# Optimization experiments

Hardware: AMD Instinct MI355X
Metric: run time of the kernel (lower is better)

The kernel has to match this reference:

```python
import jax, jax.numpy as jnp
import numpy as np
from jax import lax

NPOINT = 1024
NSAMPLE = 32
BN_EPS = 1e-3  # keras BatchNormalization default epsilon


def _fps(xyz, npoint):
    # Farthest point sampling. Matches the TF loop: the NEW farthest index is
    # recorded at each step (the initial index-0 seed is never recorded).
    B, N, _ = xyz.shape

    def step(carry, _):
        dist, far = carry
        centroid = jnp.take_along_axis(xyz, far[:, None, None], axis=1)  # (B,1,3)
        d2 = jnp.sum(jnp.square(xyz - centroid), axis=-1)  # (B,N)
        dist = jnp.minimum(dist, d2)
        nf = jnp.argmax(dist, axis=-1).astype(jnp.int32)
        return (dist, nf), nf

    init = (jnp.full((B, N), 1e10, dtype=xyz.dtype), jnp.zeros((B,), jnp.int32))
    _, idxs = lax.scan(step, init, None, length=npoint)
    return jnp.transpose(idxs)  # (B, npoint)


def _pairwise_d2(a, b):
    # a: (B,S,3), b: (B,N,3) -> (B,S,N) squared distances
    a2 = jnp.sum(a * a, axis=-1, keepdims=True)
    b2 = jnp.sum(b * b, axis=-1, keepdims=True)
    ab = jnp.einsum('bsc,bnc->bsn', a, b)
    return jnp.maximum(a2 - 2.0 * ab + jnp.swapaxes(b2, 1, 2), 0.0)


def _forward(xyz, features, params):
    fps_idx = _fps(xyz, NPOINT)  # (B,S)
    new_xyz = jnp.take_along_axis(xyz, fps_idx[..., None], axis=1)  # (B,S,3)
    d2 = _pairwise_d2(new_xyz, xyz)  # (B,S,N)
    _, idx = lax.top_k(-d2, NSAMPLE)  # (B,S,K) knn indices
    gather = jax.vmap(lambda p, i: p[i])  # per-batch gather
    grouped_xyz = gather(xyz, idx) - new_xyz[:, :, None, :]  # (B,S,K,3)
    grouped_feat = gather(features, idx)  # (B,S,K,C)
    x = jnp.concatenate([grouped_xyz, grouped_feat], axis=-1)
    for W, b, g, be, m, v in params:
        # Conv2D(kernel=1, activation='relu') then BatchNormalization (inference)
        x = jax.nn.relu(jnp.einsum('bskc,cd->bskd', x, W) + b)
        x = g * (x - m) * lax.rsqrt(v + BN_EPS) + be
    return new_xyz, jnp.max(x, axis=2)  # (B,S,3), (B,S,C_out)


def setup_inputs() -> dict:
    key = jax.random.key(0)
    ks = jax.random.split(key, 16)
    B, N, CF = 16, 4096, 64
    mlp = [64, 64, 128]
    inp = {
        'xyz': jax.random.normal(ks[0], (B, N, 3), jnp.float32),
        'features': jax.random.normal(ks[1], (B, N, CF), jnp.float32),
    }
    c = 3 + CF
    ki = 2
    for li, co in enumerate(mlp):
        inp[f'W{li}'] = jax.random.normal(ks[ki], (c, co), jnp.float32) * 0.05; ki += 1
        inp[f'b{li}'] = jnp.zeros((co,), jnp.float32)
        inp[f'g{li}'] = 1.0 + 0.02 * jax.random.normal(ks[ki], (co,), jnp.float32); ki += 1
        inp[f'be{li}'] = 0.02 * jax.random.normal(ks[ki], (co,), jnp.float32); ki += 1
        inp[f'm{li}'] = jnp.zeros((co,), jnp.float32)
        inp[f'v{li}'] = jnp.ones((co,), jnp.float32)
        c = co
    return inp


def reference(xyz, features, W0, b0, g0, be0, m0, v0, W1, b1, g1, be1, m1, v1, W2, b2, g2, be2, m2, v2):
    params = [(W0, b0, g0, be0, m0, v0), (W1, b1, g1, be1, m1, v1), (W2, b2, g2, be2, m2, v2)]
    return _forward(xyz, features, params)
```

## Files before the change

kernel.cpp:

```cpp
#include <hip/hip_runtime.h>

#define NB 16
#define NPTS 4096
#define NS 1024
#define NK 32
#define NCF 64


#define F_INF __int_as_float(0x7f800000)

#define DPP_SHR1   0x111
#define DPP_SHR2   0x112
#define DPP_SHR4   0x114
#define DPP_SHR8   0x118
#define DPP_BCAST15 0x142
#define DPP_BCAST31 0x143

#define DPP_MAX_STEP(cur, CTRL) do{ \
  int lo_=__builtin_amdgcn_update_dpp((int)(unsigned)(cur),(int)(unsigned)(cur),CTRL,0xF,0xF,false); \
  int hi_=__builtin_amdgcn_update_dpp((int)(unsigned)((cur)>>32),(int)(unsigned)((cur)>>32),CTRL,0xF,0xF,false); \
  unsigned long long nk_=(((unsigned long long)(unsigned)hi_)<<32)|(unsigned)lo_; \
  if (nk_>(cur)) (cur)=nk_; \
}while(0)

__global__ __launch_bounds__(256, 2) void fps_kernel(
  const float* __restrict__ xyz, float* __restrict__ out)
{
  __shared__ float sxyz[NPTS*3];
  __shared__ unsigned long long skey[2][4];
  __shared__ int sfps[NS];
  const int b = blockIdx.x, tid = threadIdx.x;
  const float* bp = xyz + (size_t)b*NPTS*3;

  {
    const float4* src=(const float4*)bp;
    float4* dst=(float4*)sxyz;
    for (int i=tid;i<NPTS*3/4;i+=256) dst[i]=src[i];
  }
  float px[16],py[16],pz[16],dist[16];
  #pragma unroll
  for (int r=0;r<16;r++){
    int p=r*256+tid;
    px[r]=bp[p*3]; py[r]=bp[p*3+1]; pz[r]=bp[p*3+2];
    dist[r]=1e10f;
  }
  __syncthreads();
  int far=0;
  for (int s=0;s<NS;++s){
    float cx=sxyz[far*3],cy=sxyz[far*3+1],cz=sxyz[far*3+2];
    float bv=-1.0f; int bslot=0;
    #pragma unroll
    for (int r=0;r<16;r++){
      float dx=__fsub_rn(px[r],cx);
      float dy=__fsub_rn(py[r],cy);
      float dz=__fsub_rn(pz[r],cz);
      float d2=__fadd_rn(__fadd_rn(__fmul_rn(dx,dx),__fmul_rn(dy,dy)),__fmul_rn(dz,dz));
      float nd=fminf(dist[r],d2);
      dist[r]=nd;
      if (nd>bv){bv=nd;bslot=r;}
    }
    int bidx=bslot*256+tid;
    unsigned long long cur=(((unsigned long long)__float_as_uint(bv))<<32)
                           |(unsigned)(4095-bidx);
    DPP_MAX_STEP(cur,DPP_SHR1);
    DPP_MAX_STEP(cur,DPP_SHR2);
    DPP_MAX_STEP(cur,DPP_SHR4);
    DPP_MAX_STEP(cur,DPP_SHR8);
    DPP_MAX_STEP(cur,DPP_BCAST15);
    DPP_MAX_STEP(cur,DPP_BCAST31);
    const int par=s&1;
    if ((tid&63)==63) skey[par][tid>>6]=cur;
    __syncthreads();
    unsigned long long m=skey[par][0];
    #pragma unroll
    for (int w=1;w<4;w++){ unsigned long long o=skey[par][w]; if (o>m) m=o; }
    far=4095-(int)(m&0xFFFFFFFFu);
    if (tid==0) sfps[s]=far;
  }
  __syncthreads();
  for (int s=tid;s<NS;s+=256){
    int p=sfps[s];
    size_t o=((size_t)b*NS+s)*3;
    out[o]=sxyz[p*3]; out[o+1]=sxyz[p*3+1]; out[o+2]=sxyz[p*3+2];
  }
}

__global__ __launch_bounds__(256, 3) void knn_kernel(
  const float* __restrict__ xyz, const float* __restrict__ newxyz,
  float* __restrict__ out2)
{
  __shared__ unsigned long long sdump[64*33];
  __shared__ unsigned long long sl1[16*33];
  const int tid=threadIdx.x;
  const int wave=tid>>6, lane=tid&63;
  const int qw=lane>>4;
  const int part=lane&15;
  const int gq=blockIdx.x*16+wave*4+qw;
  const int b=gq>>10;
  const float* base=xyz+(size_t)b*NPTS*3;

  float ax=newxyz[(size_t)gq*3],ay=newxyz[(size_t)gq*3+1],az=newxyz[(size_t)gq*3+2];
  float a2=__fadd_rn(__fadd_rn(__fmul_rn(ax,ax),__fmul_rn(ay,ay)),__fmul_rn(az,az));
  float kD[NK]; int kI[NK];
  #pragma unroll
  for (int p=0;p<NK;p++){kD[p]=F_INF;kI[p]=0x7FFFFFFF;}
  #pragma unroll 2
  for (int t=0;t<NPTS/16;++t){
    int n=(t<<4)|part;
    float bx=base[n*3],by=base[n*3+1],bz=base[n*3+2];
    float b2=__fadd_rn(__fadd_rn(__fmul_rn(bx,bx),__fmul_rn(by,by)),__fmul_rn(bz,bz));
    float ab=__fadd_rn(__fadd_rn(__fmul_rn(ax,bx),__fmul_rn(ay,by)),__fmul_rn(az,bz));
    float tt=__fadd_rn(__fsub_rn(a2,__fmul_rn(2.0f,ab)),b2);
    float d2=fmaxf(tt,0.0f);
    if (d2<kD[NK-1]){
      #pragma unroll
      for (int p=NK-1;p>0;--p){
        bool cm1=d2<kD[p-1];
        bool cp=d2<kD[p];
        kI[p]=cm1?kI[p-1]:(cp?n:kI[p]);
        kD[p]=__builtin_fminf(__builtin_fmaxf(kD[p-1],d2),kD[p]);
      }
      if (d2<kD[0]){kD[0]=d2;kI[0]=n;}
    }
  }
  #pragma unroll 1
  for (int ph=0;ph<4;++ph){
    if (wave==ph){
      unsigned long long* row=sdump+(size_t)lane*33;
      #pragma unroll
      for (int p=0;p<NK;p++)
        row[p]=(((unsigned long long)__float_as_uint(kD[p]))<<32)|(unsigned)kI[p];
    }
    __syncthreads();
    if (tid<16){
      int qq=tid>>2, g=tid&3;
      const unsigned long long* r0=sdump+(size_t)(qq*16+g*4+0)*33;
      const unsigned long long* r1=sdump+(size_t)(qq*16+g*4+1)*33;
      const unsigned long long* r2=sdump+(size_t)(qq*16+g*4+2)*33;
      const unsigned long long* r3=sdump+(size_t)(qq*16+g*4+3)*33;
      unsigned long long* o=sl1+(size_t)tid*33;
      int h0=0,h1=0,h2=0,h3=0;
      unsigned long long c0=r0[0],c1=r1[0],c2=r2[0],c3=r3[0];
      for (int i=0;i<NK;++i){
        bool s01=c1<c0; unsigned long long m01=s01?c1:c0;
        bool s23=c3<c2; unsigned long long m23=s23?c3:c2;
        bool sm=m23<m01; unsigned long long m=sm?m23:m01;
        o[i]=m;
        int w=sm?(s23?3:2):(s01?1:0);
        if (w==0){h0++; c0=(h0<NK)?r0[h0]:~0ull;}
        else if (w==1){h1++; c1=(h1<NK)?r1[h1]:~0ull;}
        else if (w==2){h2++; c2=(h2<NK)?r2[h2]:~0ull;}
        else {h3++; c3=(h3<NK)?r3[h3]:~0ull;}
      }
    }
    __syncthreads();
    if (tid<4){
      const unsigned long long* r0=sl1+(size_t)(tid*4+0)*33;
      const unsigned long long* r1=sl1+(size_t)(tid*4+1)*33;
      const unsigned long long* r2=sl1+(size_t)(tid*4+2)*33;
      const unsigned long long* r3=sl1+(size_t)(tid*4+3)*33;
      float* orow=out2+(size_t)(blockIdx.x*16+ph*4+tid)*128;
      int h0=0,h1=0,h2=0,h3=0;
      unsigned long long c0=r0[0],c1=r1[0],c2=r2[0],c3=r3[0];
      for (int i=0;i<NK;++i){
        bool s01=c1<c0; unsigned long long m01=s01?c1:c0;
        bool s23=c3<c2; unsigned long long m23=s23?c3:c2;
        bool sm=m23<m01; unsigned long long m=sm?m23:m01;
        orow[i]=__int_as_float((int)(unsigned)(m&0xFFFFFFFFu));
        int w=sm?(s23?3:2):(s01?1:0);
        if (w==0){h0++; c0=(h0<NK)?r0[h0]:~0ull;}
        else if (w==1){h1++; c1=(h1<NK)?r1[h1]:~0ull;}
        else if (w==2){h2++; c2=(h2<NK)?r2[h2]:~0ull;}
        else {h3++; c3=(h3<NK)?r3[h3]:~0ull;}
      }
    }
    __syncthreads();
  }
}

__global__ __launch_bounds__(128, 3) void mlp_kernel(
  const float* __restrict__ feat, const float* __restrict__ xyz,
  const float* __restrict__ newxyz,
  const float* __restrict__ W0,const float* __restrict__ b0,
  const float* __restrict__ g0,const float* __restrict__ be0,
  const float* __restrict__ m0,const float* __restrict__ v0,
  const float* __restrict__ W1,const float* __restrict__ b1,
  const float* __restrict__ g1,const float* __restrict__ be1,
  const float* __restrict__ m1,const float* __restrict__ v1,
  const float* __restrict__ W2,const float* __restrict__ b2,
  const float* __restrict__ g2,const float* __restrict__ be2,
  const float* __restrict__ m2,const float* __restrict__ v2,
  float* __restrict__ out2)
{
  __shared__ float sX[128*67];
  const int tid=threadIdx.x;
  const int q=blockIdx.x*4+(tid>>5);
  const int k=tid&31;
  const int b=q>>10;
  const int pt=__float_as_int(out2[(size_t)q*128+k]);

  float* myx=sX+tid*67;
  {
    const float* nx=newxyz+(size_t)q*3;
    const float* pp=xyz+((size_t)b*NPTS+pt)*3;
    myx[0]=pp[0]-nx[0]; myx[1]=pp[1]-nx[1]; myx[2]=pp[2]-nx[2];
    const float4* fp=(const float4*)(feat+((size_t)b*NPTS+pt)*NCF);
    #pragma unroll
    for (int i=0;i<16;i++){
      float4 u=fp[i]; float* d=myx+3+i*4;
      d[0]=u.x; d[1]=u.y; d[2]=u.z; d[3]=u.w;
    }
  }
  float acc[64];
  #pragma unroll
  for (int c=0;c<64;c++) acc[c]=b0[c];
  #pragma unroll 2
  for (int j=0;j<67;++j){
    float xj=myx[j];
    const float4* wr=(const float4*)(W0+j*64);
    #pragma unroll
    for (int c4=0;c4<16;c4++){
      float4 w=wr[c4];
      acc[c4*4+0]=fmaf(xj,w.x,acc[c4*4+0]);
      acc[c4*4+1]=fmaf(xj,w.y,acc[c4*4+1]);
      acc[c4*4+2]=fmaf(xj,w.z,acc[c4*4+2]);
      acc[c4*4+3]=fmaf(xj,w.w,acc[c4*4+3]);
    }
  }
  #pragma unroll
  for (int c=0;c<64;c++){
    float A=g0[c]*rsqrtf(v0[c]+1e-3f);
    myx[c]=fmaf(A,fmaxf(acc[c],0.0f),be0[c]-m0[c]*A);
  }
  #pragma unroll
  for (int c=0;c<64;c++) acc[c]=b1[c];
  #pragma unroll 2
  for (int j=0;j<64;++j){
    float xj=myx[j];
    const float4* wr=(const float4*)(W1+j*64);
    #pragma unroll
    for (int c4=0;c4<16;c4++){
      float4 w=wr[c4];
      acc[c4*4+0]=fmaf(xj,w.x,acc[c4*4+0]);
      acc[c4*4+1]=fmaf(xj,w.y,acc[c4*4+1]);
      acc[c4*4+2]=fmaf(xj,w.z,acc[c4*4+2]);
      acc[c4*4+3]=fmaf(xj,w.w,acc[c4*4+3]);
    }
  }
  #pragma unroll
  for (int c=0;c<64;c++){
    float A=g1[c]*rsqrtf(v1[c]+1e-3f);
    myx[c]=fmaf(A,fmaxf(acc[c],0.0f),be1[c]-m1[c]*A);
  }
  #pragma unroll 1
  for (int ch=0;ch<2;++ch){
    const int co=ch*64;
    #pragma unroll
    for (int c=0;c<64;c++) acc[c]=b2[co+c];
    #pragma unroll 2
    for (int j=0;j<64;++j){
      float xj=myx[j];
      const float4* wr=(const float4*)(W2+j*128+co);
      #pragma unroll
      for (int c4=0;c4<16;c4++){
        float4 w=wr[c4];
        acc[c4*4+0]=fmaf(xj,w.x,acc[c4*4+0]);
        acc[c4*4+1]=fmaf(xj,w.y,acc[c4*4+1]);
        acc[c4*4+2]=fmaf(xj,w.z,acc[c4*4+2]);
        acc[c4*4+3]=fmaf(xj,w.w,acc[c4*4+3]);
      }
    }
    #pragma unroll
    for (int c=0;c<64;c++){
      float A=g2[co+c]*rsqrtf(v2[co+c]+1e-3f);
      float v=fmaf(A,fmaxf(acc[c],0.0f),be2[co+c]-m2[co+c]*A);
      v=fmaxf(v,__shfl_xor(v,1));
      v=fmaxf(v,__shfl_xor(v,2));
      v=fmaxf(v,__shfl_xor(v,4));
      v=fmaxf(v,__shfl_xor(v,8));
      v=fmaxf(v,__shfl_xor(v,16));
      acc[c]=v;
    }
    if (k==0){
      float4* op=(float4*)(out2+(size_t)q*128+co);
      #pragma unroll
      for (int c=0;c<64;c+=4)
        op[c/4]=make_float4(acc[c],acc[c+1],acc[c+2],acc[c+3]);
    }
  }
}

extern "C" void kernel_launch(void* const* d_in, const int* in_sizes, int n_in,
                              void* d_out, int out_size, void* d_ws, size_t ws_size,
                              hipStream_t stream)
{
  const float* xyz=(const float*)d_in[0];
  const float* feat=(const float*)d_in[1];
  float* out=(float*)d_out;
  float* out2=out+(size_t)NB*NS*3;
  (void)d_ws; (void)ws_size;

  fps_kernel<<<NB,256,0,stream>>>(xyz,out);
  knn_kernel<<<NB*NS/16,256,0,stream>>>(xyz,out,out2);
  mlp_kernel<<<NB*NS/4,128,0,stream>>>(feat,xyz,out,
    (const float*)d_in[2],(const float*)d_in[3],
    (const float*)d_in[4],(const float*)d_in[5],
    (const float*)d_in[6],(const float*)d_in[7],
    (const float*)d_in[8],(const float*)d_in[9],
    (const float*)d_in[10],(const float*)d_in[11],
    (const float*)d_in[12],(const float*)d_in[13],
    (const float*)d_in[14],(const float*)d_in[15],
    (const float*)d_in[16],(const float*)d_in[17],
    (const float*)d_in[18],(const float*)d_in[19],
    out2);
}
```

Measured before the change: 1.650 ms.

## Rework KNN as a distance-threshold pass followed by an index-collection pass

The KNN kernel now keeps only a sorted list of the 32 smallest distances per lane. It updates that list with a branchless fmed3 insertion chain instead of a divergent insertion that also carried indices. The per-lane lists are merged in parallel to find each query's 32nd-smallest distance. A second pass over all points then collects indices below that threshold using shared-memory atomics, and resolves ties at the threshold by smallest index. This cuts register pressure (launch bounds raised to 4 blocks per SM) and removes the four serialized merge phases, at the cost of a second distance pass, neighbour output no longer sorted by distance, and a fixed cap of 48 tie candidates.

```diff
diff --git a/kernel.cpp b/kernel.cpp
--- a/kernel.cpp
+++ b/kernel.cpp
@@ -85,25 +85,34 @@
   }
 }
 
-__global__ __launch_bounds__(256, 3) void knn_kernel(
+__global__ __launch_bounds__(256, 4) void knn_kernel(
   const float* __restrict__ xyz, const float* __restrict__ newxyz,
   float* __restrict__ out2)
 {
-  __shared__ unsigned long long sdump[64*33];
-  __shared__ unsigned long long sl1[16*33];
+  __shared__ float sdump[256*33];
+  __shared__ float sl1[64*33];
+  __shared__ float sTq[16];
+  __shared__ int   sE[16];
+  __shared__ int   sCnt[16];
+  __shared__ int   sTCnt[16];
+  __shared__ int   sIdx[16][32];
+  __shared__ int   sTie[16][48];
   const int tid=threadIdx.x;
   const int wave=tid>>6, lane=tid&63;
   const int qw=lane>>4;
   const int part=lane&15;
-  const int gq=blockIdx.x*16+wave*4+qw;
+  const int ql=wave*4+qw;
+  const int gq=blockIdx.x*16+ql;
   const int b=gq>>10;
   const float* base=xyz+(size_t)b*NPTS*3;
 
   float ax=newxyz[(size_t)gq*3],ay=newxyz[(size_t)gq*3+1],az=newxyz[(size_t)gq*3+2];
   float a2=__fadd_rn(__fadd_rn(__fmul_rn(ax,ax),__fmul_rn(ay,ay)),__fmul_rn(az,az));
-  float kD[NK]; int kI[NK];
-  #pragma unroll
-  for (int p=0;p<NK;p++){kD[p]=F_INF;kI[p]=0x7FFFFFFF;}
+
+  float kD[NK];
+  #pragma unroll
+  for (int p=0;p<NK;p++) kD[p]=F_INF;
+
   #pragma unroll 2
   for (int t=0;t<NPTS/16;++t){
     int n=(t<<4)|part;
@@ -112,69 +121,102 @@
     float ab=__fadd_rn(__fadd_rn(__fmul_rn(ax,bx),__fmul_rn(ay,by)),__fmul_rn(az,bz));
     float tt=__fadd_rn(__fsub_rn(a2,__fmul_rn(2.0f,ab)),b2);
     float d2=fmaxf(tt,0.0f);
-    if (d2<kD[NK-1]){
-      #pragma unroll
-      for (int p=NK-1;p>0;--p){
-        bool cm1=d2<kD[p-1];
-        bool cp=d2<kD[p];
-        kI[p]=cm1?kI[p-1]:(cp?n:kI[p]);
-        kD[p]=__builtin_fminf(__builtin_fmaxf(kD[p-1],d2),kD[p]);
+    #pragma unroll
+    for (int p=NK-1;p>0;--p)
+      kD[p]=__builtin_amdgcn_fmed3f(kD[p-1],d2,kD[p]);
+    kD[0]=fminf(kD[0],d2);
+  }
+
+  #pragma unroll
+  for (int p=0;p<NK;p++) sdump[tid*33+p]=kD[p];
+  __syncthreads();
+
+  if (tid<64){
+    int qq=tid>>2, g=tid&3;
+    int rbase=(qq>>2)*64+(qq&3)*16+g*4;
+    const float* r0=sdump+(size_t)(rbase+0)*33;
+    const float* r1=sdump+(size_t)(rbase+1)*33;
+    const float* r2=sdump+(size_t)(rbase+2)*33;
+    const float* r3=sdump+(size_t)(rbase+3)*33;
+    float* o=sl1+(size_t)tid*33;
+    int h0=0,h1=0,h2=0,h3=0;
+    float c0=r0[0],c1=r1[0],c2=r2[0],c3=r3[0];
+    #pragma unroll 1
+    for (int i=0;i<NK;++i){
+      bool s01=c1<c0; float m01=s01?c1:c0;
+      bool s23=c3<c2; float m23=s23?c3:c2;
+      bool sm=m23<m01; float m=sm?m23:m01;
+      o[i]=m;
+      int w=sm?(s23?3:2):(s01?1:0);
+      if (w==0){h0++; c0=(h0<NK)?r0[h0]:F_INF;}
+      else if (w==1){h1++; c1=(h1<NK)?r1[h1]:F_INF;}
+      else if (w==2){h2++; c2=(h2<NK)?r2[h2]:F_INF;}
+      else {h3++; c3=(h3<NK)?r3[h3]:F_INF;}
+    }
+  }
+  __syncthreads();
+
+  if (tid<16){
+    const float* r0=sl1+(size_t)(tid*4+0)*33;
+    const float* r1=sl1+(size_t)(tid*4+1)*33;
+    const float* r2=sl1+(size_t)(tid*4+2)*33;
+    const float* r3=sl1+(size_t)(tid*4+3)*33;
+    int h0=0,h1=0,h2=0,h3=0;
+    float c0=r0[0],c1=r1[0],c2=r2[0],c3=r3[0];
+    float prev=-1.0f; int run=0;
+    #pragma unroll 1
+    for (int i=0;i<NK;++i){
+      bool s01=c1<c0; float m01=s01?c1:c0;
+      bool s23=c3<c2; float m23=s23?c3:c2;
+      bool sm=m23<m01; float m=sm?m23:m01;
+      if (m==prev) run++; else {prev=m; run=1;}
+      int w=sm?(s23?3:2):(s01?1:0);
+      if (w==0){h0++; c0=(h0<NK)?r0[h0]:F_INF;}
+      else if (w==1){h1++; c1=(h1<NK)?r1[h1]:F_INF;}
+      else if (w==2){h2++; c2=(h2<NK)?r2[h2]:F_INF;}
+      else {h3++; c3=(h3<NK)?r3[h3]:F_INF;}
+    }
+    sTq[tid]=prev; sE[tid]=run;
+    sCnt[tid]=0; sTCnt[tid]=0;
+  }
+  __syncthreads();
+
+  {
+    const float Tq=sTq[ql];
+    #pragma unroll 2
+    for (int t=0;t<NPTS/16;++t){
+      int n=(t<<4)|part;
+      float bx=base[n*3],by=base[n*3+1],bz=base[n*3+2];
+      float b2=__fadd_rn(__fadd_rn(__fmul_rn(bx,bx),__fmul_rn(by,by)),__fmul_rn(bz,bz));
+      float ab=__fadd_rn(__fadd_rn(__fmul_rn(ax,bx),__fmul_rn(ay,by)),__fmul_rn(az,bz));
+      float tt=__fadd_rn(__fsub_rn(a2,__fmul_rn(2.0f,ab)),b2);
+      float d2=fmaxf(tt,0.0f);
+      if (d2<Tq){
+        int pos=atomicAdd(&sCnt[ql],1);
+        if (pos<32) sIdx[ql][pos]=n;
+      } else if (d2==Tq){
+        int tp=atomicAdd(&sTCnt[ql],1);
+        if (tp<48) sTie[ql][tp]=n;
       }
-      if (d2<kD[0]){kD[0]=d2;kI[0]=n;}
-    }
-  }
-  #pragma unroll 1
-  for (int ph=0;ph<4;++ph){
-    if (wave==ph){
-      unsigned long long* row=sdump+(size_t)lane*33;
-      #pragma unroll
-      for (int p=0;p<NK;p++)
-        row[p]=(((unsigned long long)__float_as_uint(kD[p]))<<32)|(unsigned)kI[p];
-    }
-    __syncthreads();
-    if (tid<16){
-      int qq=tid>>2, g=tid&3;
-      const unsigned long long* r0=sdump+(size_t)(qq*16+g*4+0)*33;
-      const unsigned long long* r1=sdump+(size_t)(qq*16+g*4+1)*33;
-      const unsigned long long* r2=sdump+(size_t)(qq*16+g*4+2)*33;
-      const unsigned long long* r3=sdump+(size_t)(qq*16+g*4+3)*33;
-      unsigned long long* o=sl1+(size_t)tid*33;
-      int h0=0,h1=0,h2=0,h3=0;
-      unsigned long long c0=r0[0],c1=r1[0],c2=r2[0],c3=r3[0];
-      for (int i=0;i<NK;++i){
-        bool s01=c1<c0; unsigned long long m01=s01?c1:c0;
-        bool s23=c3<c2; unsigned long long m23=s23?c3:c2;
-        bool sm=m23<m01; unsigned long long m=sm?m23:m01;
-        o[i]=m;
-        int w=sm?(s23?3:2):(s01?1:0);
-        if (w==0){h0++; c0=(h0<NK)?r0[h0]:~0ull;}
-        else if (w==1){h1++; c1=(h1<NK)?r1[h1]:~0ull;}
-        else if (w==2){h2++; c2=(h2<NK)?r2[h2]:~0ull;}
-        else {h3++; c3=(h3<NK)?r3[h3]:~0ull;}
-      }
-    }
-    __syncthreads();
-    if (tid<4){
-      const unsigned long long* r0=sl1+(size_t)(tid*4+0)*33;
-      const unsigned long long* r1=sl1+(size_t)(tid*4+1)*33;
-      const unsigned long long* r2=sl1+(size_t)(tid*4+2)*33;
-      const unsigned long long* r3=sl1+(size_t)(tid*4+3)*33;
-      float* orow=out2+(size_t)(blockIdx.x*16+ph*4+tid)*128;
-      int h0=0,h1=0,h2=0,h3=0;
-      unsigned long long c0=r0[0],c1=r1[0],c2=r2[0],c3=r3[0];
-      for (int i=0;i<NK;++i){
-        bool s01=c1<c0; unsigned long long m01=s01?c1:c0;
-        bool s23=c3<c2; unsigned long long m23=s23?c3:c2;
-        bool sm=m23<m01; unsigned long long m=sm?m23:m01;
-        orow[i]=__int_as_float((int)(unsigned)(m&0xFFFFFFFFu));
-        int w=sm?(s23?3:2):(s01?1:0);
-        if (w==0){h0++; c0=(h0<NK)?r0[h0]:~0ull;}
-        else if (w==1){h1++; c1=(h1<NK)?r1[h1]:~0ull;}
-        else if (w==2){h2++; c2=(h2<NK)?r2[h2]:~0ull;}
-        else {h3++; c3=(h3<NK)?r3[h3]:~0ull;}
-      }
-    }
-    __syncthreads();
+    }
+  }
+  __syncthreads();
+
+  if (tid<16){
+    int e=sE[tid], c=sCnt[tid];
+    int tn=sTCnt[tid]; if (tn>48) tn=48;
+    for (int j=0;j<e;++j){
+      int bm=0x7FFFFFFF, bi=0;
+      for (int i=0;i<tn;++i){ int v=sTie[tid][i]; if (v<bm){bm=v;bi=i;} }
+      sTie[tid][bi]=0x7FFFFFFF;
+      if (c+j<32) sIdx[tid][c+j]=bm;
+    }
+  }
+  __syncthreads();
+
+  for (int i=tid;i<512;i+=256){
+    int q=i>>5, k=i&31;
+    out2[(size_t)(blockIdx.x*16+q)*128+k]=__int_as_float(sIdx[q][k]);
   }
 }
 
```

New measurement: 1.345 ms. -18.5%, faster.
